# Optimization experiments

Hardware: AMD Instinct MI355X
Metric: run time of the kernel (lower is better)

## Reference

```python
import jax, jax.numpy as jnp
import numpy as np

D_MODEL = 1024
D_STATE = 512
SEQ_LEN = 16384
R_MIN, R_MAX, MAX_PHASE = 0.0, 1.0, 6.28


def setup_inputs() -> dict:
    key = jax.random.key(0)
    ks = jax.random.split(key, 8)
    inputs = jax.random.normal(ks[0], (SEQ_LEN, D_MODEL), dtype=jnp.float32)
    # parameter init exactly as in the module
    u_nu = jax.random.uniform(ks[1], (D_STATE,), dtype=jnp.float32)
    nu_log = jnp.log(-0.5 * jnp.log(u_nu * (R_MAX ** 2 - R_MIN ** 2) + R_MIN ** 2))
    u_th = jax.random.uniform(ks[2], (D_STATE,), dtype=jnp.float32)
    theta_log = jnp.log(MAX_PHASE * u_th)
    diag_lambda = jnp.exp(-jnp.exp(nu_log) + 1j * jnp.exp(theta_log))
    gamma_log = jnp.log(jnp.sqrt(1.0 - jnp.abs(diag_lambda) ** 2))
    bn = jnp.sqrt(jnp.asarray(2 * D_MODEL, jnp.float32))
    cn = jnp.sqrt(jnp.asarray(D_STATE, jnp.float32))
    B_re = jax.random.normal(ks[3], (D_STATE, D_MODEL), dtype=jnp.float32) / bn
    B_im = jax.random.normal(ks[4], (D_STATE, D_MODEL), dtype=jnp.float32) / bn
    C_re = jax.random.normal(ks[5], (D_MODEL, D_STATE), dtype=jnp.float32) / cn
    C_im = jax.random.normal(ks[6], (D_MODEL, D_STATE), dtype=jnp.float32) / cn
    D = jax.random.normal(ks[7], (D_MODEL,), dtype=jnp.float32)
    return {"inputs": inputs, "nu_log": nu_log, "theta_log": theta_log,
            "gamma_log": gamma_log, "B_re": B_re, "B_im": B_im,
            "C_re": C_re, "C_im": C_im, "D": D}


def _binop(q_i, q_j):
    # associative combine for diagonal linear recurrence h' = a*h + b
    a_i, b_i = q_i
    a_j, b_j = q_j
    return (a_j * a_i, a_j * b_i + b_j)


def reference(inputs, nu_log, theta_log, gamma_log, B_re, B_im, C_re, C_im, D):
    L = inputs.shape[0]
    diag_lambda = jnp.exp(-jnp.exp(nu_log) + 1j * jnp.exp(theta_log))  # (d_state,)
    B_norm = (B_re + 1j * B_im) * jnp.exp(gamma_log)[:, None]          # (d_state, d_model)
    C = C_re + 1j * C_im                                               # (d_model, d_state)
    # Bu[t] = B_norm @ x_t  -> (L, d_state) complex
    Bu = inputs.astype(B_norm.dtype) @ B_norm.T
    Lambda_elems = jnp.broadcast_to(diag_lambda, (L, diag_lambda.shape[0]))
    _, h = jax.lax.associative_scan(_binop, (Lambda_elems, Bu))        # (L, d_state)
    # y_t = Re[C h_t] + D * x_t
    return jnp.real(h @ C.T) + D * inputs
```

## Files before the change

### kernel.cpp

```cpp
#include <hip/hip_runtime.h>
#include <math.h>

#define L_SEQ   16384
#define DMODEL  1024
#define NST     512
#define CHUNK   128
#define NCHUNK  (L_SEQ / CHUNK)

typedef float  f32x4 __attribute__((ext_vector_type(4)));
typedef short  s16x8 __attribute__((ext_vector_type(8)));

__device__ __forceinline__ unsigned short f2bf(float f) {
    union { float f; unsigned int u; } v; v.f = f;
    unsigned int r = v.u + 0x7fffu + ((v.u >> 16) & 1u);
    return (unsigned short)(r >> 16);
}
__device__ __forceinline__ unsigned short f2bf_fast(float f) {
    union { float f; unsigned int u; } v; v.f = f;
    return (unsigned short)((v.u + 0x8000u) >> 16);
}
__device__ __forceinline__ float bf2f(unsigned int h16) {
    union { unsigned int u; float f; } v; v.u = h16 << 16; return v.f;
}
__device__ __forceinline__ void mfma16(f32x4& d, s16x8 a, s16x8 b) {
    asm volatile("v_mfma_f32_16x16x32_bf16 %0, %1, %2, %0"
                 : "+v"(d) : "v"(a), "v"(b));
}
__device__ __forceinline__ uint4 pack8(float4 x, float4 y) {
    union { unsigned short u[8]; uint4 v; } t;
    t.u[0] = f2bf_fast(x.x); t.u[1] = f2bf_fast(x.y);
    t.u[2] = f2bf_fast(x.z); t.u[3] = f2bf_fast(x.w);
    t.u[4] = f2bf_fast(y.x); t.u[5] = f2bf_fast(y.y);
    t.u[6] = f2bf_fast(y.z); t.u[7] = f2bf_fast(y.w);
    return t.v;
}
__device__ __forceinline__ void gload16(const unsigned short* g, unsigned short* l) {
    __builtin_amdgcn_global_load_lds(
        (const __attribute__((address_space(1))) unsigned int*)g,
        (__attribute__((address_space(3))) unsigned int*)l,
        16, 0, 0);
}

__global__ void setup_params(const float* __restrict__ nu_log,
                             const float* __restrict__ theta_log,
                             const float* __restrict__ gamma_log,
                             float* __restrict__ lam,
                             float* __restrict__ lamT,
                             float* __restrict__ gam) {
    int s = threadIdx.x;
    if (s >= NST) return;
    float mod = expf(-expf(nu_log[s]));
    float th  = expf(theta_log[s]);
    float ar = mod * cosf(th);
    float ai = mod * sinf(th);
    lam[s] = ar; lam[NST + s] = ai;
    gam[s] = expf(gamma_log[s]);
    float pr = 1.f, pi = 0.f;
    for (int i = 0; i < CHUNK; ++i) {
        float nr = pr * ar - pi * ai;
        float ni = pr * ai + pi * ar;
        pr = nr; pi = ni;
    }
    lamT[s] = pr; lamT[NST + s] = pi;
}

__global__ void pack_w1(const float* __restrict__ Bre, const float* __restrict__ Bim,
                        unsigned short* __restrict__ W1) {
    int idx = blockIdx.x * 256 + threadIdx.x;
    int n = idx >> 10, k = idx & 1023;
    int s = n >> 1;
    float v = (n & 1) ? Bim[s * DMODEL + k] : Bre[s * DMODEL + k];
    W1[idx] = f2bf(v);
}
__global__ void pack_w2(const float* __restrict__ Cre, const float* __restrict__ Cim,
                        unsigned short* __restrict__ W2) {
    int idx = blockIdx.x * 256 + threadIdx.x;
    int n = idx >> 10, k = idx & 1023;
    int s = k >> 1;
    float v = (k & 1) ? -Cim[n * NST + s] : Cre[n * NST + s];
    W2[idx] = f2bf(v);
}

__global__ __launch_bounds__(256)
void conv_x(const float4* __restrict__ X, uint4* __restrict__ Xb) {
    int i = blockIdx.x * 256 + threadIdx.x;
    float4 a = X[2 * i], b = X[2 * i + 1];
    Xb[i] = pack8(a, b);
}

template<int EPI>
__global__ __launch_bounds__(256)
void gemm_bf16(const unsigned short* __restrict__ A, const unsigned short* __restrict__ B,
               void* __restrict__ out, const float* __restrict__ Dv,
               const float* __restrict__ Xf) {
    const int K = 1024, N = 1024;
    __shared__ __align__(16) unsigned short As[128 * 32];
    __shared__ __align__(16) unsigned short Bs[128 * 32];

    const int tid  = threadIdx.x;
    const int lane = tid & 63;
    const int wave = tid >> 6;
    const int wr   = wave >> 1, wc = wave & 1;

    const int lin   = blockIdx.y * gridDim.x + blockIdx.x;
    const int n_new = (lin & 7) * 128 + (lin >> 3);
    const int bx = n_new & 7, by = n_new >> 3;
    const int m0 = by * 128, n0 = bx * 128;

    const int srow = tid >> 2;
    const int skb  = (tid & 3) * 8;

    const unsigned short* Ag0 = A + (size_t)(m0 + srow) * K + skb;
    const unsigned short* Ag1 = Ag0 + (size_t)64 * K;
    const unsigned short* Bg0 = B + (size_t)(n0 + srow) * K + skb;
    const unsigned short* Bg1 = Bg0 + (size_t)64 * K;

    unsigned short* Ad0 = &As[tid * 8];
    unsigned short* Ad1 = &As[2048 + tid * 8];
    unsigned short* Bd0 = &Bs[tid * 8];
    unsigned short* Bd1 = &Bs[2048 + tid * 8];

    f32x4 acc[4][4] = {};

    const int fr = lane & 15;
    const int fk = (lane >> 4) * 8;

    for (int k0 = 0; k0 < K; k0 += 32) {
        __syncthreads();
        gload16(Ag0 + k0, Ad0);
        gload16(Ag1 + k0, Ad1);
        gload16(Bg0 + k0, Bd0);
        gload16(Bg1 + k0, Bd1);
        __syncthreads();

        s16x8 af[4], bfq[4];
        #pragma unroll
        for (int i = 0; i < 4; ++i)
            af[i] = *(const s16x8*)&As[(wr * 64 + i * 16 + fr) * 32 + fk];
        #pragma unroll
        for (int j = 0; j < 4; ++j)
            bfq[j] = *(const s16x8*)&Bs[(wc * 64 + j * 16 + fr) * 32 + fk];
        #pragma unroll
        for (int i = 0; i < 4; ++i)
            #pragma unroll
            for (int j = 0; j < 4; ++j)
                mfma16(acc[i][j], af[i], bfq[j]);
    }

    const int crow = (lane >> 4) * 4;
    const int ccol = lane & 15;
    #pragma unroll
    for (int i = 0; i < 4; ++i) {
        #pragma unroll
        for (int j = 0; j < 4; ++j) {
            const int mbase = m0 + wr * 64 + i * 16 + crow;
            const int n     = n0 + wc * 64 + j * 16 + ccol;
            #pragma unroll
            for (int r = 0; r < 4; ++r) {
                const int m = mbase + r;
                if (EPI) {
                    ((float*)out)[(size_t)m * N + n] =
                        acc[i][j][r] + Dv[n] * Xf[(size_t)m * N + n];
                } else {
                    ((unsigned short*)out)[(size_t)m * N + n] = f2bf(acc[i][j][r]);
                }
            }
        }
    }
}

__global__ __launch_bounds__(128)
void scan_ends(const unsigned int* __restrict__ Bu, const float* __restrict__ lam,
               const float* __restrict__ gam, float* __restrict__ ends) {
    const int s = blockIdx.y * 128 + threadIdx.x;
    const int c = blockIdx.x;
    const float lr = lam[s], li = lam[NST + s], g = gam[s];
    float hr = 0.f, hi = 0.f;
    size_t base = (size_t)c * CHUNK * NST + s;
    #pragma unroll 4
    for (int t = 0; t < CHUNK; ++t) {
        unsigned int v = Bu[base + (size_t)t * NST];
        float br = g * bf2f(v & 0xffffu);
        float bi = g * bf2f(v >> 16);
        float nr = fmaf(lr, hr, fmaf(-li, hi, br));
        float ni = fmaf(lr, hi, fmaf( li, hr, bi));
        hr = nr; hi = ni;
    }
    ends[(size_t)(c * NST + s) * 2]     = hr;
    ends[(size_t)(c * NST + s) * 2 + 1] = hi;
}

__global__ __launch_bounds__(NST)
void scan_carry(const float* __restrict__ ends, const float* __restrict__ lamT,
                float* __restrict__ car) {
    const int s = threadIdx.x;
    const float ar = lamT[s], ai = lamT[NST + s];
    float cr = 0.f, ci = 0.f;
    for (int c = 0; c < NCHUNK; ++c) {
        car[(size_t)(c * NST + s) * 2]     = cr;
        car[(size_t)(c * NST + s) * 2 + 1] = ci;
        float er = ends[(size_t)(c * NST + s) * 2];
        float ei = ends[(size_t)(c * NST + s) * 2 + 1];
        float nr = fmaf(ar, cr, fmaf(-ai, ci, er));
        float ni = fmaf(ar, ci, fmaf( ai, cr, ei));
        cr = nr; ci = ni;
    }
}

__global__ __launch_bounds__(128)
void scan_h(const unsigned int* __restrict__ Bu, unsigned int* __restrict__ H,
            const float* __restrict__ lam, const float* __restrict__ gam,
            const float* __restrict__ car) {
    const int s = blockIdx.y * 128 + threadIdx.x;
    const int c = blockIdx.x;
    const float lr = lam[s], li = lam[NST + s], g = gam[s];
    float hr = car[(size_t)(c * NST + s) * 2];
    float hi = car[(size_t)(c * NST + s) * 2 + 1];
    size_t base = (size_t)c * CHUNK * NST + s;
    #pragma unroll 4
    for (int t = 0; t < CHUNK; ++t) {
        unsigned int v = Bu[base + (size_t)t * NST];
        float br = g * bf2f(v & 0xffffu);
        float bi = g * bf2f(v >> 16);
        float nr = fmaf(lr, hr, fmaf(-li, hi, br));
        float ni = fmaf(lr, hi, fmaf( li, hr, bi));
        hr = nr; hi = ni;
        H[base + (size_t)t * NST] =
            (unsigned int)f2bf(hr) | ((unsigned int)f2bf(hi) << 16);
    }
}

extern "C" void kernel_launch(void* const* d_in, const int* in_sizes, int n_in,
                              void* d_out, int out_size, void* d_ws, size_t ws_size,
                              hipStream_t stream) {
    const float* X         = (const float*)d_in[0];
    const float* nu_log    = (const float*)d_in[1];
    const float* theta_log = (const float*)d_in[2];
    const float* gamma_log = (const float*)d_in[3];
    const float* Bre       = (const float*)d_in[4];
    const float* Bim       = (const float*)d_in[5];
    const float* Cre       = (const float*)d_in[6];
    const float* Cim       = (const float*)d_in[7];
    const float* Dv        = (const float*)d_in[8];
    float* Y = (float*)d_out;

    char* ws = (char*)d_ws;
    size_t off = 0;
    unsigned short* Xb  = (unsigned short*)(ws + off); off += (size_t)L_SEQ * DMODEL * 2;
    unsigned short* H   = Xb;
    unsigned short* W1  = (unsigned short*)(ws + off); off += (size_t)DMODEL * DMODEL * 2;
    unsigned short* W2  = (unsigned short*)(ws + off); off += (size_t)DMODEL * DMODEL * 2;
    float* lam  = (float*)(ws + off); off += 1024 * 4;
    float* lamT = (float*)(ws + off); off += 1024 * 4;
    float* gam  = (float*)(ws + off); off += 512 * 4;
    float* ends = (float*)(ws + off); off += (size_t)NCHUNK * NST * 2 * 4;
    float* car  = (float*)(ws + off); off += (size_t)NCHUNK * NST * 2 * 4;
    unsigned short* Bu = (unsigned short*)d_out;

    setup_params<<<1, NST, 0, stream>>>(nu_log, theta_log, gamma_log, lam, lamT, gam);
    pack_w1<<<(DMODEL * DMODEL) / 256, 256, 0, stream>>>(Bre, Bim, W1);
    pack_w2<<<(DMODEL * DMODEL) / 256, 256, 0, stream>>>(Cre, Cim, W2);
    conv_x<<<(L_SEQ * DMODEL / 8) / 256, 256, 0, stream>>>((const float4*)X, (uint4*)Xb);

    dim3 gg(8, 128);
    gemm_bf16<0><<<gg, 256, 0, stream>>>(Xb, W1, Bu, nullptr, nullptr);

    dim3 gs(NCHUNK, 4);
    scan_ends<<<gs, 128, 0, stream>>>((const unsigned int*)Bu, lam, gam, ends);
    scan_carry<<<1, NST, 0, stream>>>(ends, lamT, car);
    scan_h<<<gs, 128, 0, stream>>>((const unsigned int*)Bu, (unsigned int*)H, lam, gam, car);

    gemm_bf16<1><<<gg, 256, 0, stream>>>(H, W2, Y, Dv, X);
}
```

Baseline: 175.3 us.

## Replace GEMM with 256x256-tile double-buffered 8-wave pipelined kernel

Replaces the 128x128 single-buffered bf16 GEMM with a 256x256-tile, 512-thread kernel. It double-buffers 64-wide K slices in LDS with an XOR swizzle and prefetches the next slice with direct global-to-LDS loads while MFMAs run. Compute phases are split by barriers and raised wave priority. The aim is to hide global load latency, cut LDS bank conflicts, and raise data reuse per block. In exchange it uses 128KB of LDS and a large accumulator, which limits occupancy to one block per CU with 256 blocks.

Measured after the change: 170.0 us. 3.0% less time.

```diff
diff --git a/kernel.cpp b/kernel.cpp
--- a/kernel.cpp
+++ b/kernel.cpp
@@ -6,6 +6,7 @@
 #define NST     512
 #define CHUNK   128
 #define NCHUNK  (L_SEQ / CHUNK)
+#define NT      16
 
 typedef float  f32x4 __attribute__((ext_vector_type(4)));
 typedef short  s16x8 __attribute__((ext_vector_type(8)));
@@ -39,6 +40,11 @@
         (const __attribute__((address_space(1))) unsigned int*)g,
         (__attribute__((address_space(3))) unsigned int*)l,
         16, 0, 0);
+}
+__device__ __forceinline__ void bar() {
+    asm volatile("" ::: "memory");
+    __builtin_amdgcn_s_barrier();
+    asm volatile("" ::: "memory");
 }
 
 __global__ void setup_params(const float* __restrict__ nu_log,
@@ -88,81 +94,114 @@
     Xb[i] = pack8(a, b);
 }
 
+
+#define DO_TILE(BUF, T)                                                          \
+  {                                                                              \
+    _Pragma("unroll")                                                            \
+    for (int q = 0; q < 4; ++q) {                                                \
+      if ((q & 1) == 0) {                                                        \
+        _Pragma("unroll")                                                        \
+        for (int i = 0; i < 4; ++i) {                                            \
+          const int arow = wr * 128 + ((q >> 1) * 4 + i) * 16 + fr;              \
+          _Pragma("unroll")                                                      \
+          for (int kx = 0; kx < 2; ++kx)                                         \
+            af[i][kx] = *(const s16x8*)                                          \
+                &lds[BUF][0][arow * 64 + (((kx * 4 + g4) ^ f7) << 3)];           \
+        }                                                                        \
+      }                                                                          \
+      s16x8 bfr[2][2];                                                           \
+      _Pragma("unroll")                                                          \
+      for (int j = 0; j < 2; ++j) {                                              \
+        const int brow = wc * 64 + ((q & 1) * 2 + j) * 16 + fr;                  \
+        _Pragma("unroll")                                                        \
+        for (int kx = 0; kx < 2; ++kx)                                           \
+          bfr[j][kx] = *(const s16x8*)                                           \
+              &lds[BUF][1][brow * 64 + (((kx * 4 + g4) ^ f7) << 3)];             \
+      }                                                                          \
+      if (q == 0 && (T) + 1 < NT) {                                              \
+        const size_t ksrc = (size_t)((T) + 1) * 64;                              \
+        _Pragma("unroll")                                                        \
+        for (int j = 0; j < 4; ++j) {                                            \
+          gload16(Asrc + (size_t)(64 * j) * 1024 + ksrc,                         \
+                  &lds[BUF ^ 1][0][j * 4096 + tid * 8]);                         \
+          gload16(Bsrc + (size_t)(64 * j) * 1024 + ksrc,                         \
+                  &lds[BUF ^ 1][1][j * 4096 + tid * 8]);                         \
+        }                                                                        \
+      }                                                                          \
+      bar();                                                                     \
+      __builtin_amdgcn_s_setprio(1);                                             \
+      _Pragma("unroll")                                                          \
+      for (int kx = 0; kx < 2; ++kx)                                             \
+        _Pragma("unroll")                                                        \
+        for (int i = 0; i < 4; ++i)                                              \
+          _Pragma("unroll")                                                      \
+          for (int j = 0; j < 2; ++j)                                            \
+            mfma16(acc[(q >> 1) * 4 + i][(q & 1) * 2 + j], af[i][kx], bfr[j][kx]); \
+      __builtin_amdgcn_s_setprio(0);                                             \
+      if (q == 3) asm volatile("s_waitcnt vmcnt(0)" ::: "memory");               \
+      bar();                                                                     \
+    }                                                                            \
+  }
+
 template<int EPI>
-__global__ __launch_bounds__(256)
-void gemm_bf16(const unsigned short* __restrict__ A, const unsigned short* __restrict__ B,
-               void* __restrict__ out, const float* __restrict__ Dv,
-               const float* __restrict__ Xf) {
-    const int K = 1024, N = 1024;
-    __shared__ __align__(16) unsigned short As[128 * 32];
-    __shared__ __align__(16) unsigned short Bs[128 * 32];
+__global__ __launch_bounds__(512)
+void gemm_8ph(const unsigned short* __restrict__ A, const unsigned short* __restrict__ Bm,
+              void* __restrict__ out, const float* __restrict__ Dv,
+              const float* __restrict__ Xf) {
+    __shared__ unsigned short lds[2][2][16384];
 
     const int tid  = threadIdx.x;
     const int lane = tid & 63;
     const int wave = tid >> 6;
-    const int wr   = wave >> 1, wc = wave & 1;
-
-    const int lin   = blockIdx.y * gridDim.x + blockIdx.x;
-    const int n_new = (lin & 7) * 128 + (lin >> 3);
-    const int bx = n_new & 7, by = n_new >> 3;
-    const int m0 = by * 128, n0 = bx * 128;
-
-    const int srow = tid >> 2;
-    const int skb  = (tid & 3) * 8;
-
-    const unsigned short* Ag0 = A + (size_t)(m0 + srow) * K + skb;
-    const unsigned short* Ag1 = Ag0 + (size_t)64 * K;
-    const unsigned short* Bg0 = B + (size_t)(n0 + srow) * K + skb;
-    const unsigned short* Bg1 = Bg0 + (size_t)64 * K;
-
-    unsigned short* Ad0 = &As[tid * 8];
-    unsigned short* Ad1 = &As[2048 + tid * 8];
-    unsigned short* Bd0 = &Bs[tid * 8];
-    unsigned short* Bd1 = &Bs[2048 + tid * 8];
-
-    f32x4 acc[4][4] = {};
-
-    const int fr = lane & 15;
-    const int fk = (lane >> 4) * 8;
-
-    for (int k0 = 0; k0 < K; k0 += 32) {
-        __syncthreads();
-        gload16(Ag0 + k0, Ad0);
-        gload16(Ag1 + k0, Ad1);
-        gload16(Bg0 + k0, Bd0);
-        gload16(Bg1 + k0, Bd1);
-        __syncthreads();
-
-        s16x8 af[4], bfq[4];
-        #pragma unroll
-        for (int i = 0; i < 4; ++i)
-            af[i] = *(const s16x8*)&As[(wr * 64 + i * 16 + fr) * 32 + fk];
-        #pragma unroll
-        for (int j = 0; j < 4; ++j)
-            bfq[j] = *(const s16x8*)&Bs[(wc * 64 + j * 16 + fr) * 32 + fk];
-        #pragma unroll
-        for (int i = 0; i < 4; ++i)
-            #pragma unroll
-            for (int j = 0; j < 4; ++j)
-                mfma16(acc[i][j], af[i], bfq[j]);
+    const int wr   = wave >> 2;
+    const int wc   = wave & 3;
+    const int fr   = lane & 15;
+    const int g4   = lane >> 4;
+    const int f7   = fr & 7;
+
+    const int lin   = blockIdx.x;
+    const int n_new = (lin & 7) * 32 + (lin >> 3);
+    const int bx = n_new & 3, by = n_new >> 2;
+    const int m0 = by * 256, n0 = bx * 256;
+
+    const int srow_in = tid >> 3;
+    const int skc     = tid & 7;
+    const int kc_src  = skc ^ (srow_in & 7);
+    const unsigned short* Asrc = A  + (size_t)(m0 + srow_in) * 1024 + kc_src * 8;
+    const unsigned short* Bsrc = Bm + (size_t)(n0 + srow_in) * 1024 + kc_src * 8;
+
+    f32x4 acc[8][4] = {};
+    s16x8 af[4][2];
+
+    #pragma unroll
+    for (int j = 0; j < 4; ++j) {
+        gload16(Asrc + (size_t)(64 * j) * 1024, &lds[0][0][j * 4096 + tid * 8]);
+        gload16(Bsrc + (size_t)(64 * j) * 1024, &lds[0][1][j * 4096 + tid * 8]);
+    }
+    asm volatile("s_waitcnt vmcnt(0)" ::: "memory");
+    bar();
+
+    for (int tt = 0; tt < NT; tt += 2) {
+        DO_TILE(0, tt)
+        DO_TILE(1, tt + 1)
     }
 
     const int crow = (lane >> 4) * 4;
     const int ccol = lane & 15;
     #pragma unroll
-    for (int i = 0; i < 4; ++i) {
+    for (int mf = 0; mf < 8; ++mf) {
         #pragma unroll
         for (int j = 0; j < 4; ++j) {
-            const int mbase = m0 + wr * 64 + i * 16 + crow;
-            const int n     = n0 + wc * 64 + j * 16 + ccol;
+            const int n  = n0 + wc * 64 + j * 16 + ccol;
+            const int mb = m0 + wr * 128 + mf * 16 + crow;
             #pragma unroll
             for (int r = 0; r < 4; ++r) {
-                const int m = mbase + r;
+                const int m = mb + r;
                 if (EPI) {
-                    ((float*)out)[(size_t)m * N + n] =
-                        acc[i][j][r] + Dv[n] * Xf[(size_t)m * N + n];
+                    ((float*)out)[(size_t)m * 1024 + n] =
+                        acc[mf][j][r] + Dv[n] * Xf[(size_t)m * 1024 + n];
                 } else {
-                    ((unsigned short*)out)[(size_t)m * N + n] = f2bf(acc[i][j][r]);
+                    ((unsigned short*)out)[(size_t)m * 1024 + n] = f2bf(acc[mf][j][r]);
                 }
             }
         }
@@ -262,13 +301,12 @@
     pack_w2<<<(DMODEL * DMODEL) / 256, 256, 0, stream>>>(Cre, Cim, W2);
     conv_x<<<(L_SEQ * DMODEL / 8) / 256, 256, 0, stream>>>((const float4*)X, (uint4*)Xb);
 
-    dim3 gg(8, 128);
-    gemm_bf16<0><<<gg, 256, 0, stream>>>(Xb, W1, Bu, nullptr, nullptr);
+    gemm_8ph<0><<<256, 512, 0, stream>>>(Xb, W1, Bu, nullptr, nullptr);
 
     dim3 gs(NCHUNK, 4);
     scan_ends<<<gs, 128, 0, stream>>>((const unsigned int*)Bu, lam, gam, ends);
     scan_carry<<<1, NST, 0, stream>>>(ends, lamT, car);
     scan_h<<<gs, 128, 0, stream>>>((const unsigned int*)Bu, (unsigned int*)H, lam, gam, car);
 
-    gemm_bf16<1><<<gg, 256, 0, stream>>>(H, W2, Y, Dv, X);
-}
+    gemm_8ph<1><<<256, 512, 0, stream>>>(H, W2, Y, Dv, X);
+}
```

## Stage GEMM epilogues through LDS, re-layout LDS tiles, prefetch carry scan

Applied to the files above, without the earlier changes.

The GEMM now loads A/B tiles in a k-group-major LDS layout so fragment reads are contiguous per 16-lane group. Both epilogues stage the accumulators through shared memory and then write rows with 16-byte vector stores, applying the D*x FMA with float4 loads. Before, each thread scattered scalar stores. The serial carry scan now double-buffers its loads of the chunk ends into registers and uses float2 accesses, so the load latency on its serial chain is hidden. The cost is extra barriers and LDS traffic in the epilogue.

After: 253.8 us. +44.8%, slower.

```diff
diff --git a/kernel.cpp b/kernel.cpp
--- a/kernel.cpp
+++ b/kernel.cpp
@@ -94,8 +94,9 @@
                void* __restrict__ out, const float* __restrict__ Dv,
                const float* __restrict__ Xf) {
     const int K = 1024, N = 1024;
-    __shared__ __align__(16) unsigned short As[128 * 32];
-    __shared__ __align__(16) unsigned short Bs[128 * 32];
+    __shared__ __align__(16) unsigned short sm[8192];
+    unsigned short* As = sm;
+    unsigned short* Bs = sm + 4096;
 
     const int tid  = threadIdx.x;
     const int lane = tid & 63;
@@ -107,39 +108,30 @@
     const int bx = n_new & 7, by = n_new >> 3;
     const int m0 = by * 128, n0 = bx * 128;
 
-    const int srow = tid >> 2;
-    const int skb  = (tid & 3) * 8;
-
-    const unsigned short* Ag0 = A + (size_t)(m0 + srow) * K + skb;
-    const unsigned short* Ag1 = Ag0 + (size_t)64 * K;
-    const unsigned short* Bg0 = B + (size_t)(n0 + srow) * K + skb;
-    const unsigned short* Bg1 = Bg0 + (size_t)64 * K;
-
-    unsigned short* Ad0 = &As[tid * 8];
-    unsigned short* Ad1 = &As[2048 + tid * 8];
-    unsigned short* Bd0 = &Bs[tid * 8];
-    unsigned short* Bd1 = &Bs[2048 + tid * 8];
+    const int arow  = tid & 127;
+    const int ahalf = tid >> 7;
+    const unsigned short* Asrc = A + (size_t)(m0 + arow) * K + ahalf * 8;
+    const unsigned short* Bsrc = B + (size_t)(n0 + arow) * K + ahalf * 8;
 
     f32x4 acc[4][4] = {};
-
     const int fr = lane & 15;
-    const int fk = (lane >> 4) * 8;
+    const int g4 = lane >> 4;
 
     for (int k0 = 0; k0 < K; k0 += 32) {
         __syncthreads();
-        gload16(Ag0 + k0, Ad0);
-        gload16(Ag1 + k0, Ad1);
-        gload16(Bg0 + k0, Bd0);
-        gload16(Bg1 + k0, Bd1);
+        gload16(Asrc + k0,      &As[tid * 8]);
+        gload16(Asrc + k0 + 16, &As[2048 + tid * 8]);
+        gload16(Bsrc + k0,      &Bs[tid * 8]);
+        gload16(Bsrc + k0 + 16, &Bs[2048 + tid * 8]);
         __syncthreads();
 
         s16x8 af[4], bfq[4];
         #pragma unroll
         for (int i = 0; i < 4; ++i)
-            af[i] = *(const s16x8*)&As[(wr * 64 + i * 16 + fr) * 32 + fk];
+            af[i] = *(const s16x8*)&As[g4 * 1024 + (wr * 64 + i * 16 + fr) * 8];
         #pragma unroll
         for (int j = 0; j < 4; ++j)
-            bfq[j] = *(const s16x8*)&Bs[(wc * 64 + j * 16 + fr) * 32 + fk];
+            bfq[j] = *(const s16x8*)&Bs[g4 * 1024 + (wc * 64 + j * 16 + fr) * 8];
         #pragma unroll
         for (int i = 0; i < 4; ++i)
             #pragma unroll
@@ -147,23 +139,62 @@
                 mfma16(acc[i][j], af[i], bfq[j]);
     }
 
-    const int crow = (lane >> 4) * 4;
-    const int ccol = lane & 15;
-    #pragma unroll
-    for (int i = 0; i < 4; ++i) {
-        #pragma unroll
-        for (int j = 0; j < 4; ++j) {
-            const int mbase = m0 + wr * 64 + i * 16 + crow;
-            const int n     = n0 + wc * 64 + j * 16 + ccol;
+    const int crow = g4 * 4;
+    const int ccol = fr;
+
+    if (EPI == 0) {
+        #pragma unroll
+        for (int p = 0; p < 2; ++p) {
+            __syncthreads();
+            if (wr == p) {
+                #pragma unroll
+                for (int i = 0; i < 4; ++i)
+                    #pragma unroll
+                    for (int j = 0; j < 4; ++j)
+                        #pragma unroll
+                        for (int r = 0; r < 4; ++r)
+                            sm[(i * 16 + crow + r) * 128 + wc * 64 + j * 16 + ccol]
+                                = f2bf(acc[i][j][r]);
+            }
+            __syncthreads();
+            const int row = tid >> 2, cq = (tid & 3) * 32;
+            const uint4* src = (const uint4*)&sm[row * 128 + cq];
+            uint4 v0 = src[0], v1 = src[1], v2 = src[2], v3 = src[3];
+            uint4* dst = (uint4*)&((unsigned short*)out)[(size_t)(m0 + p * 64 + row) * N + n0 + cq];
+            dst[0] = v0; dst[1] = v1; dst[2] = v2; dst[3] = v3;
+        }
+    } else {
+        float* smf = (float*)sm;
+        #pragma unroll
+        for (int p = 0; p < 4; ++p) {
+            __syncthreads();
+            if (wr == (p >> 1)) {
+                const int ib = (p & 1) * 2;
+                #pragma unroll
+                for (int ii = 0; ii < 2; ++ii)
+                    #pragma unroll
+                    for (int j = 0; j < 4; ++j)
+                        #pragma unroll
+                        for (int r = 0; r < 4; ++r)
+                            smf[(ii * 16 + crow + r) * 128 + wc * 64 + j * 16 + ccol]
+                                = acc[ib + ii][j][r];
+            }
+            __syncthreads();
+            const int row = tid >> 3;
+            const int cf  = (tid & 7) * 16;
+            const int m   = m0 + p * 32 + row;
+            const float4* sp = (const float4*)&smf[row * 128 + cf];
+            const float4* xp = (const float4*)&Xf[(size_t)m * N + n0 + cf];
+            const float4* dp = (const float4*)&Dv[n0 + cf];
+            float4*       yp = (float4*)&((float*)out)[(size_t)m * N + n0 + cf];
             #pragma unroll
-            for (int r = 0; r < 4; ++r) {
-                const int m = mbase + r;
-                if (EPI) {
-                    ((float*)out)[(size_t)m * N + n] =
-                        acc[i][j][r] + Dv[n] * Xf[(size_t)m * N + n];
-                } else {
-                    ((unsigned short*)out)[(size_t)m * N + n] = f2bf(acc[i][j][r]);
-                }
+            for (int q = 0; q < 4; ++q) {
+                float4 v = sp[q], xv = xp[q], dv = dp[q], o;
+                o.x = fmaf(dv.x, xv.x, v.x);
+                o.y = fmaf(dv.y, xv.y, v.y);
+                o.z = fmaf(dv.z, xv.z, v.z);
+                o.w = fmaf(dv.w, xv.w, v.w);
+                yp[q] = o;
             }
         }
     }
@@ -195,15 +226,37 @@
                 float* __restrict__ car) {
     const int s = threadIdx.x;
     const float ar = lamT[s], ai = lamT[NST + s];
+    const float2* E = (const float2*)ends;
+    float2*       C = (float2*)car;
+    float2 bufA[8], bufB[8];
+    #pragma unroll
+    for (int k = 0; k < 8; ++k) bufA[k] = E[(size_t)k * NST + s];
     float cr = 0.f, ci = 0.f;
-    for (int c = 0; c < NCHUNK; ++c) {
-        car[(size_t)(c * NST + s) * 2]     = cr;
-        car[(size_t)(c * NST + s) * 2 + 1] = ci;
-        float er = ends[(size_t)(c * NST + s) * 2];
-        float ei = ends[(size_t)(c * NST + s) * 2 + 1];
-        float nr = fmaf(ar, cr, fmaf(-ai, ci, er));
-        float ni = fmaf(ar, ci, fmaf( ai, cr, ei));
-        cr = nr; ci = ni;
+    for (int cc = 0; cc < NCHUNK; cc += 16) {
+        #pragma unroll
+        for (int k = 0; k < 8; ++k)
+            bufB[k] = E[(size_t)(cc + 8 + k) * NST + s];
+        #pragma unroll
+        for (int k = 0; k < 8; ++k) {
+            float2 o; o.x = cr; o.y = ci;
+            C[(size_t)(cc + k) * NST + s] = o;
+            float nr = fmaf(ar, cr, fmaf(-ai, ci, bufA[k].x));
+            float ni = fmaf(ar, ci, fmaf( ai, cr, bufA[k].y));
+            cr = nr; ci = ni;
+        }
+        if (cc + 16 < NCHUNK) {
+            #pragma unroll
+            for (int k = 0; k < 8; ++k)
+                bufA[k] = E[(size_t)(cc + 16 + k) * NST + s];
+        }
+        #pragma unroll
+        for (int k = 0; k < 8; ++k) {
+            float2 o; o.x = cr; o.y = ci;
+            C[(size_t)(cc + 8 + k) * NST + s] = o;
+            float nr = fmaf(ar, cr, fmaf(-ai, ci, bufB[k].x));
+            float ni = fmaf(ar, ci, fmaf( ai, cr, bufB[k].y));
+            cr = nr; ci = ni;
+        }
     }
 }
 
```

## Widen GEMM K-tile with swizzled LDS and prefetch carry scan loads

Applied to the files above, without the earlier changes.

The GEMM K-step doubles from 32 to 64, with an XOR-swizzled LDS layout that avoids bank conflicts on fragment reads, and launch bounds now request 4 blocks per CU. This halves the number of barrier pairs per tile and cuts LDS conflicts, at the cost of doubled shared memory per block. The serial carry scan now loads chunk ends as float2 into register buffers prefetched 8 ahead, hiding global load latency on its dependent chain.

Measured after the change: 164.4 us. 1.07x faster.

```diff
diff --git a/kernel.cpp b/kernel.cpp
--- a/kernel.cpp
+++ b/kernel.cpp
@@ -89,66 +89,66 @@
 }
 
 template<int EPI>
-__global__ __launch_bounds__(256)
+__global__ __launch_bounds__(256, 4)
 void gemm_bf16(const unsigned short* __restrict__ A, const unsigned short* __restrict__ B,
                void* __restrict__ out, const float* __restrict__ Dv,
                const float* __restrict__ Xf) {
     const int K = 1024, N = 1024;
-    __shared__ __align__(16) unsigned short As[128 * 32];
-    __shared__ __align__(16) unsigned short Bs[128 * 32];
+    __shared__ __align__(16) unsigned short As[128 * 64];
+    __shared__ __align__(16) unsigned short Bs[128 * 64];
 
     const int tid  = threadIdx.x;
     const int lane = tid & 63;
     const int wave = tid >> 6;
     const int wr   = wave >> 1, wc = wave & 1;
+    const int fr   = lane & 15;
+    const int g4   = lane >> 4;
+    const int f7   = fr & 7;
 
     const int lin   = blockIdx.y * gridDim.x + blockIdx.x;
     const int n_new = (lin & 7) * 128 + (lin >> 3);
     const int bx = n_new & 7, by = n_new >> 3;
     const int m0 = by * 128, n0 = bx * 128;
 
-    const int srow = tid >> 2;
-    const int skb  = (tid & 3) * 8;
-
-    const unsigned short* Ag0 = A + (size_t)(m0 + srow) * K + skb;
-    const unsigned short* Ag1 = Ag0 + (size_t)64 * K;
-    const unsigned short* Bg0 = B + (size_t)(n0 + srow) * K + skb;
-    const unsigned short* Bg1 = Bg0 + (size_t)64 * K;
-
-    unsigned short* Ad0 = &As[tid * 8];
-    unsigned short* Ad1 = &As[2048 + tid * 8];
-    unsigned short* Bd0 = &Bs[tid * 8];
-    unsigned short* Bd1 = &Bs[2048 + tid * 8];
+    const int srow   = tid >> 3;
+    const int schunk = (tid & 7) ^ (srow & 7);
+    const unsigned short* Asrc = A + (size_t)(m0 + srow) * K + schunk * 8;
+    const unsigned short* Bsrc = B + (size_t)(n0 + srow) * K + schunk * 8;
 
     f32x4 acc[4][4] = {};
 
-    const int fr = lane & 15;
-    const int fk = (lane >> 4) * 8;
-
-    for (int k0 = 0; k0 < K; k0 += 32) {
+    for (int k0 = 0; k0 < K; k0 += 64) {
         __syncthreads();
-        gload16(Ag0 + k0, Ad0);
-        gload16(Ag1 + k0, Ad1);
-        gload16(Bg0 + k0, Bd0);
-        gload16(Bg1 + k0, Bd1);
+        #pragma unroll
+        for (int ld = 0; ld < 4; ++ld) {
+            gload16(Asrc + (size_t)(ld * 32) * K + k0, &As[ld * 2048 + tid * 8]);
+            gload16(Bsrc + (size_t)(ld * 32) * K + k0, &Bs[ld * 2048 + tid * 8]);
+        }
         __syncthreads();
 
-        s16x8 af[4], bfq[4];
-        #pragma unroll
-        for (int i = 0; i < 4; ++i)
-            af[i] = *(const s16x8*)&As[(wr * 64 + i * 16 + fr) * 32 + fk];
-        #pragma unroll
-        for (int j = 0; j < 4; ++j)
-            bfq[j] = *(const s16x8*)&Bs[(wc * 64 + j * 16 + fr) * 32 + fk];
-        #pragma unroll
-        for (int i = 0; i < 4; ++i)
-            #pragma unroll
-            for (int j = 0; j < 4; ++j)
-                mfma16(acc[i][j], af[i], bfq[j]);
-    }
-
-    const int crow = (lane >> 4) * 4;
-    const int ccol = lane & 15;
+        #pragma unroll
+        for (int h = 0; h < 2; ++h) {
+            s16x8 af[4], bfq[4];
+            #pragma unroll
+            for (int i = 0; i < 4; ++i) {
+                const int row = wr * 64 + i * 16 + fr;
+                af[i] = *(const s16x8*)&As[row * 64 + (((h * 4 + g4) ^ f7) << 3)];
+            }
+            #pragma unroll
+            for (int j = 0; j < 4; ++j) {
+                const int row = wc * 64 + j * 16 + fr;
+                bfq[j] = *(const s16x8*)&Bs[row * 64 + (((h * 4 + g4) ^ f7) << 3)];
+            }
+            #pragma unroll
+            for (int i = 0; i < 4; ++i)
+                #pragma unroll
+                for (int j = 0; j < 4; ++j)
+                    mfma16(acc[i][j], af[i], bfq[j]);
+        }
+    }
+
+    const int crow = g4 * 4;
+    const int ccol = fr;
     #pragma unroll
     for (int i = 0; i < 4; ++i) {
         #pragma unroll
@@ -195,15 +195,37 @@
                 float* __restrict__ car) {
     const int s = threadIdx.x;
     const float ar = lamT[s], ai = lamT[NST + s];
+    const float2* E = (const float2*)ends;
+    float2*       C = (float2*)car;
+    float2 bufA[8], bufB[8];
+    #pragma unroll
+    for (int k = 0; k < 8; ++k) bufA[k] = E[(size_t)k * NST + s];
     float cr = 0.f, ci = 0.f;
-    for (int c = 0; c < NCHUNK; ++c) {
-        car[(size_t)(c * NST + s) * 2]     = cr;
-        car[(size_t)(c * NST + s) * 2 + 1] = ci;
-        float er = ends[(size_t)(c * NST + s) * 2];
-        float ei = ends[(size_t)(c * NST + s) * 2 + 1];
-        float nr = fmaf(ar, cr, fmaf(-ai, ci, er));
-        float ni = fmaf(ar, ci, fmaf( ai, cr, ei));
-        cr = nr; ci = ni;
+    for (int cc = 0; cc < NCHUNK; cc += 16) {
+        #pragma unroll
+        for (int k = 0; k < 8; ++k)
+            bufB[k] = E[(size_t)(cc + 8 + k) * NST + s];
+        #pragma unroll
+        for (int k = 0; k < 8; ++k) {
+            float2 o; o.x = cr; o.y = ci;
+            C[(size_t)(cc + k) * NST + s] = o;
+            float nr = fmaf(ar, cr, fmaf(-ai, ci, bufA[k].x));
+            float ni = fmaf(ar, ci, fmaf( ai, cr, bufA[k].y));
+            cr = nr; ci = ni;
+        }
+        if (cc + 16 < NCHUNK) {
+            #pragma unroll
+            for (int k = 0; k < 8; ++k)
+                bufA[k] = E[(size_t)(cc + 16 + k) * NST + s];
+        }
+        #pragma unroll
+        for (int k = 0; k < 8; ++k) {
+            float2 o; o.x = cr; o.y = ci;
+            C[(size_t)(cc + 8 + k) * NST + s] = o;
+            float nr = fmaf(ar, cr, fmaf(-ai, ci, bufB[k].x));
+            float ni = fmaf(ar, ci, fmaf( ai, cr, bufB[k].y));
+            cr = nr; ci = ni;
+        }
     }
 }
 
```
